# Kernel optimization log

Measured on AMD Instinct MI355X. Metric: run time of the kernel, lower is better.

Reference implementation:

```python
import jax, jax.numpy as jnp
from jax import lax
import numpy as np

T, B, H = 128, 4096, 64

def setup_inputs() -> dict:
    key = jax.random.key(0)
    ks = jax.random.split(key, 7)
    s = 1.0 / np.sqrt(H)
    Hseq = jax.random.normal(ks[0], (T, B, H), dtype=jnp.float32)
    # PyTorch nn.GRU params: weight_ih_l0 [3H,H], weight_hh_l0 [3H,H], biases [3H]; gate order r,z,n
    W_ih = jax.random.uniform(ks[1], (3 * H, H), jnp.float32, -s, s)
    W_hh = jax.random.uniform(ks[2], (3 * H, H), jnp.float32, -s, s)
    b_ih = jax.random.uniform(ks[3], (3 * H,), jnp.float32, -s, s)
    b_hh = jax.random.uniform(ks[4], (3 * H,), jnp.float32, -s, s)
    W_out = jax.random.uniform(ks[5], (1, H), jnp.float32, -s, s)
    b_out = jax.random.uniform(ks[6], (1,), jnp.float32, -s, s)
    return {"Hseq": Hseq, "W_ih": W_ih, "W_hh": W_hh, "b_ih": b_ih, "b_hh": b_hh, "W_out": W_out, "b_out": b_out}

def reference(Hseq, W_ih, W_hh, b_ih, b_hh, W_out, b_out):
    # Precompute all input-side gate projections in one big GEMM: [T,B,3H]
    x_gates = jnp.einsum('tbh,gh->tbg', Hseq, W_ih) + b_ih

    def step(h, xg):
        hg = h @ W_hh.T + b_hh                     # [B,3H]
        xr, xz, xn = jnp.split(xg, 3, axis=-1)
        hr, hz, hn = jnp.split(hg, 3, axis=-1)
        r = jax.nn.sigmoid(xr + hr)
        z = jax.nn.sigmoid(xz + hz)
        n = jnp.tanh(xn + r * hn)
        h_new = (1.0 - z) * n + z * h
        return h_new, None

    h0 = jnp.zeros(Hseq.shape[1:], Hseq.dtype)      # [B,H], PyTorch default h0=0
    last, _ = lax.scan(step, h0, x_gates)           # last hidden == Y[-1]
    return (last @ W_out.T + b_out).squeeze(-1)     # [B]
```

## Files before the change

kernel.cpp:

```cpp
#include <hip/hip_runtime.h>
#include <stdint.h>

#define TT 128
#define BB 4096
#define HH 64
#define BC 16
#define XSTR 196
#define HSTR 72

typedef __attribute__((ext_vector_type(8))) short bf16x8;
typedef __attribute__((ext_vector_type(4))) float f32x4;

static __device__ __forceinline__ short f2bf(float f) {
  uint32_t u = __builtin_bit_cast(uint32_t, f);
  u += 0x7fffu + ((u >> 16) & 1u);
  return (short)(u >> 16);
}
static __device__ __forceinline__ uint32_t cvtpk(float a, float b) {
  uint32_t r;
  asm("v_cvt_pk_bf16_f32 %0, %1, %2" : "=v"(r) : "v"(a), "v"(b));
  return r;
}
static __device__ __forceinline__ float rcpf(float x) { return __builtin_amdgcn_rcpf(x); }
static __device__ __forceinline__ float sigm(float x) { return rcpf(1.0f + __expf(-x)); }
static __device__ __forceinline__ float tanhf_fast(float x) {
  float e = __expf(2.0f * x);
  return 1.0f - 2.0f * rcpf(e + 1.0f);
}

static __device__ __forceinline__ void block_sync_lds() {
  asm volatile("" ::: "memory");
  asm volatile("s_waitcnt lgkmcnt(0)" ::: "memory");
  __builtin_amdgcn_s_barrier();
  asm volatile("" ::: "memory");
}

__global__ __launch_bounds__(512) void gru_fused(
    const float* __restrict__ Hseq, const float* __restrict__ W_ih,
    const float* __restrict__ W_hh, const float* __restrict__ b_ih,
    const float* __restrict__ b_hh, const float* __restrict__ W_out,
    const float* __restrict__ b_out, float* __restrict__ out) {
  __shared__ __align__(16) short hsh[2][BC][HSTR];
  __shared__ __align__(16) float xgsh[2][BC][XSTR];
  __shared__ float psum[4][BC];

  const int tid = threadIdx.x;
  const int w   = tid >> 6;
  const int gw  = w & 3;
  const bool cons = (w < 4);
  const int l   = tid & 63;
  const int llo = l & 15;
  const int lhi = l >> 4;
  const int k0  = lhi * 8;
  const int bbase = blockIdx.x * BC;

  for (int i = tid; i < BC * HSTR; i += 512) ((short*)hsh[0])[i] = 0;

  bf16x8 wa[3][2];
  f32x4 biasHN = {0, 0, 0, 0};
  f32x4 biasPR = {0, 0, 0, 0}, biasPZ = {0, 0, 0, 0}, biasPN = {0, 0, 0, 0};
  f32x4 hfp = {0.f, 0.f, 0.f, 0.f};
  f32x4 xq0 = {0,0,0,0}, xq1 = {0,0,0,0}, xq2 = {0,0,0,0}, xq3 = {0,0,0,0};

  if (cons) {
#pragma unroll
    for (int c = 0; c < 3; ++c) {
      const int grow = 16 * gw + 64 * c + llo;
#pragma unroll
      for (int hf = 0; hf < 2; ++hf) {
        const float* q = &W_hh[grow * 64 + hf * 32 + k0];
        bf16x8 b;
#pragma unroll
        for (int i = 0; i < 8; ++i) b[i] = f2bf(q[i]);
        wa[c][hf] = b;
      }
    }
#pragma unroll
    for (int r = 0; r < 4; ++r) biasHN[r] = b_hh[128 + 16 * gw + lhi * 4 + r];
  } else {
#pragma unroll
    for (int c = 0; c < 3; ++c) {
      const int grow = 16 * gw + 64 * c + llo;
#pragma unroll
      for (int hf = 0; hf < 2; ++hf) {
        const float* p = &W_ih[grow * 64 + hf * 32 + k0];
        bf16x8 a;
#pragma unroll
        for (int i = 0; i < 8; ++i) a[i] = f2bf(p[i]);
        wa[c][hf] = a;
      }
    }
#pragma unroll
    for (int r = 0; r < 4; ++r) {
      const int j = 16 * gw + lhi * 4 + r;
      biasPR[r] = b_ih[j] + b_hh[j];
      biasPZ[r] = b_ih[64 + j] + b_hh[64 + j];
      biasPN[r] = b_ih[128 + j];
    }
    const f32x4* p = (const f32x4*)(Hseq + (size_t)(bbase + llo) * HH + k0);
    xq0 = p[0]; xq1 = p[1]; xq2 = p[8]; xq3 = p[9];
  }

  if (!cons) {
    union { uint32_t u[4]; bf16x8 v; } c0, c1;
    c0.u[0] = cvtpk(xq0[0], xq0[1]); c0.u[1] = cvtpk(xq0[2], xq0[3]);
    c0.u[2] = cvtpk(xq1[0], xq1[1]); c0.u[3] = cvtpk(xq1[2], xq1[3]);
    c1.u[0] = cvtpk(xq2[0], xq2[1]); c1.u[1] = cvtpk(xq2[2], xq2[3]);
    c1.u[2] = cvtpk(xq3[0], xq3[1]); c1.u[3] = cvtpk(xq3[2], xq3[3]);
    f32x4 cR = biasPR, cZ = biasPZ, cN = biasPN;
    cR = __builtin_amdgcn_mfma_f32_16x16x32_bf16(wa[0][0], c0.v, cR, 0, 0, 0);
    cR = __builtin_amdgcn_mfma_f32_16x16x32_bf16(wa[0][1], c1.v, cR, 0, 0, 0);
    cZ = __builtin_amdgcn_mfma_f32_16x16x32_bf16(wa[1][0], c0.v, cZ, 0, 0, 0);
    cZ = __builtin_amdgcn_mfma_f32_16x16x32_bf16(wa[1][1], c1.v, cZ, 0, 0, 0);
    cN = __builtin_amdgcn_mfma_f32_16x16x32_bf16(wa[2][0], c0.v, cN, 0, 0, 0);
    cN = __builtin_amdgcn_mfma_f32_16x16x32_bf16(wa[2][1], c1.v, cN, 0, 0, 0);
    *(f32x4*)&xgsh[0][llo][16 * gw + lhi * 4]       = cR;
    *(f32x4*)&xgsh[0][llo][64 + 16 * gw + lhi * 4]  = cZ;
    *(f32x4*)&xgsh[0][llo][128 + 16 * gw + lhi * 4] = cN;
    const f32x4* p = (const f32x4*)(Hseq + ((size_t)BB + bbase + llo) * HH + k0);
    xq0 = p[0]; xq1 = p[1]; xq2 = p[8]; xq3 = p[9];
  }
  block_sync_lds();

  for (int t = 0; t < TT; ++t) {
    const int buf = t & 1;
    if (cons) {
      f32x4 aR  = *(const f32x4*)&xgsh[buf][llo][16 * gw + lhi * 4];
      f32x4 aZ  = *(const f32x4*)&xgsh[buf][llo][64 + 16 * gw + lhi * 4];
      f32x4 aXN = *(const f32x4*)&xgsh[buf][llo][128 + 16 * gw + lhi * 4];
      f32x4 aHN = biasHN;
      const bf16x8 hb0 = *(const bf16x8*)&hsh[buf][llo][k0];
      const bf16x8 hb1 = *(const bf16x8*)&hsh[buf][llo][k0 + 32];
      aR  = __builtin_amdgcn_mfma_f32_16x16x32_bf16(wa[0][0], hb0, aR, 0, 0, 0);
      aR  = __builtin_amdgcn_mfma_f32_16x16x32_bf16(wa[0][1], hb1, aR, 0, 0, 0);
      aZ  = __builtin_amdgcn_mfma_f32_16x16x32_bf16(wa[1][0], hb0, aZ, 0, 0, 0);
      aZ  = __builtin_amdgcn_mfma_f32_16x16x32_bf16(wa[1][1], hb1, aZ, 0, 0, 0);
      aHN = __builtin_amdgcn_mfma_f32_16x16x32_bf16(wa[2][0], hb0, aHN, 0, 0, 0);
      aHN = __builtin_amdgcn_mfma_f32_16x16x32_bf16(wa[2][1], hb1, aHN, 0, 0, 0);
#pragma unroll
      for (int r = 0; r < 4; ++r) {
        const float rr = sigm(aR[r]);
        const float zz = sigm(aZ[r]);
        const float nn = tanhf_fast(aXN[r] + rr * aHN[r]);
        hfp[r] = (1.0f - zz) * nn + zz * hfp[r];
      }
      uint2 pk;
      pk.x = cvtpk(hfp[0], hfp[1]);
      pk.y = cvtpk(hfp[2], hfp[3]);
      *(uint2*)&hsh[buf ^ 1][llo][16 * gw + lhi * 4] = pk;
    } else {
      union { uint32_t u[4]; bf16x8 v; } c0, c1;
      c0.u[0] = cvtpk(xq0[0], xq0[1]); c0.u[1] = cvtpk(xq0[2], xq0[3]);
      c0.u[2] = cvtpk(xq1[0], xq1[1]); c0.u[3] = cvtpk(xq1[2], xq1[3]);
      c1.u[0] = cvtpk(xq2[0], xq2[1]); c1.u[1] = cvtpk(xq2[2], xq2[3]);
      c1.u[2] = cvtpk(xq3[0], xq3[1]); c1.u[3] = cvtpk(xq3[2], xq3[3]);
      const int tn = (t + 2 < TT) ? t + 2 : TT - 1;
      const f32x4* p = (const f32x4*)(Hseq + ((size_t)tn * BB + bbase + llo) * HH + k0);
      xq0 = p[0]; xq1 = p[1]; xq2 = p[8]; xq3 = p[9];
      f32x4 cR = biasPR, cZ = biasPZ, cN = biasPN;
      cR = __builtin_amdgcn_mfma_f32_16x16x32_bf16(wa[0][0], c0.v, cR, 0, 0, 0);
      cR = __builtin_amdgcn_mfma_f32_16x16x32_bf16(wa[0][1], c1.v, cR, 0, 0, 0);
      cZ = __builtin_amdgcn_mfma_f32_16x16x32_bf16(wa[1][0], c0.v, cZ, 0, 0, 0);
      cZ = __builtin_amdgcn_mfma_f32_16x16x32_bf16(wa[1][1], c1.v, cZ, 0, 0, 0);
      cN = __builtin_amdgcn_mfma_f32_16x16x32_bf16(wa[2][0], c0.v, cN, 0, 0, 0);
      cN = __builtin_amdgcn_mfma_f32_16x16x32_bf16(wa[2][1], c1.v, cN, 0, 0, 0);
      const int ob = buf ^ 1;
      *(f32x4*)&xgsh[ob][llo][16 * gw + lhi * 4]       = cR;
      *(f32x4*)&xgsh[ob][llo][64 + 16 * gw + lhi * 4]  = cZ;
      *(f32x4*)&xgsh[ob][llo][128 + 16 * gw + lhi * 4] = cN;
    }
    block_sync_lds();
  }

  if (cons) {
    float part = 0.f;
#pragma unroll
    for (int r = 0; r < 4; ++r) part += hfp[r] * W_out[16 * gw + lhi * 4 + r];
    part += __shfl_xor(part, 16);
    part += __shfl_xor(part, 32);
    if (lhi == 0) psum[gw][llo] = part;
  }
  block_sync_lds();
  if (tid < BC)
    out[bbase + tid] = psum[0][tid] + psum[1][tid] + psum[2][tid] + psum[3][tid] + b_out[0];
}

extern "C" void kernel_launch(void* const* d_in, const int* in_sizes, int n_in,
                              void* d_out, int out_size, void* d_ws, size_t ws_size,
                              hipStream_t stream) {
  (void)in_sizes; (void)n_in; (void)d_ws; (void)ws_size; (void)out_size;
  const float* Hseq  = (const float*)d_in[0];
  const float* W_ih  = (const float*)d_in[1];
  const float* W_hh  = (const float*)d_in[2];
  const float* b_ih  = (const float*)d_in[3];
  const float* b_hh  = (const float*)d_in[4];
  const float* W_out = (const float*)d_in[5];
  const float* b_out = (const float*)d_in[6];
  float* out = (float*)d_out;
  gru_fused<<<BB / BC, 512, 0, stream>>>(Hseq, W_ih, W_hh, b_ih, b_hh, W_out, b_out, out);
}
```

Before: 71.42 us.

## Unroll GRU recurrence by two, deepen input prefetch, fuse gate math, raise consumer priority

The time loop is unrolled by two with constant LDS buffer indices. The producer warps now prefetch two timesteps ahead using two register sets, which hides global load latency better. The consumer gate math is rewritten so the z-sigmoid, tanh and blend collapse into a single reciprocal, with clamps to avoid overflow, which cuts transcendental and rcp count on the serial critical path. Consumer warps raise their scheduling priority with s_setprio so the latency-bound recurrence is favored over producer work. The cost is higher register pressure, and the algebraic rewrite could change numerics slightly at extreme values.

```diff
diff --git a/kernel.cpp b/kernel.cpp
--- a/kernel.cpp
+++ b/kernel.cpp
@@ -22,11 +22,6 @@
   return r;
 }
 static __device__ __forceinline__ float rcpf(float x) { return __builtin_amdgcn_rcpf(x); }
-static __device__ __forceinline__ float sigm(float x) { return rcpf(1.0f + __expf(-x)); }
-static __device__ __forceinline__ float tanhf_fast(float x) {
-  float e = __expf(2.0f * x);
-  return 1.0f - 2.0f * rcpf(e + 1.0f);
-}
 
 static __device__ __forceinline__ void block_sync_lds() {
   asm volatile("" ::: "memory");
@@ -34,6 +29,8 @@
   __builtin_amdgcn_s_barrier();
   asm volatile("" ::: "memory");
 }
+
+#define MFMA __builtin_amdgcn_mfma_f32_16x16x32_bf16
 
 __global__ __launch_bounds__(512) void gru_fused(
     const float* __restrict__ Hseq, const float* __restrict__ W_ih,
@@ -59,8 +56,6 @@
   bf16x8 wa[3][2];
   f32x4 biasHN = {0, 0, 0, 0};
   f32x4 biasPR = {0, 0, 0, 0}, biasPZ = {0, 0, 0, 0}, biasPN = {0, 0, 0, 0};
-  f32x4 hfp = {0.f, 0.f, 0.f, 0.f};
-  f32x4 xq0 = {0,0,0,0}, xq1 = {0,0,0,0}, xq2 = {0,0,0,0}, xq3 = {0,0,0,0};
 
   if (cons) {
 #pragma unroll
@@ -76,7 +71,7 @@
       }
     }
 #pragma unroll
-    for (int r = 0; r < 4; ++r) biasHN[r] = b_hh[128 + 16 * gw + lhi * 4 + r];
+    for (int r = 0; r < 4; ++r) biasHN[r] = b_hh[128 + 16 * gw + 4 * lhi + r];
   } else {
 #pragma unroll
     for (int c = 0; c < 3; ++c) {
@@ -92,90 +87,114 @@
     }
 #pragma unroll
     for (int r = 0; r < 4; ++r) {
-      const int j = 16 * gw + lhi * 4 + r;
+      const int j = 16 * gw + 4 * lhi + r;
       biasPR[r] = b_ih[j] + b_hh[j];
       biasPZ[r] = b_ih[64 + j] + b_hh[64 + j];
       biasPN[r] = b_ih[128 + j];
     }
-    const f32x4* p = (const f32x4*)(Hseq + (size_t)(bbase + llo) * HH + k0);
-    xq0 = p[0]; xq1 = p[1]; xq2 = p[8]; xq3 = p[9];
-  }
+  }
+
+  const float* xroot = Hseq + (size_t)(bbase + llo) * HH + k0;
+  f32x4 xqA0, xqA1, xqA2, xqA3, xqB0, xqB1, xqB2, xqB3;
+  f32x4 hfp = {0.f, 0.f, 0.f, 0.f};
 
   if (!cons) {
+    const f32x4* pv = (const f32x4*)xroot;
+    f32x4 q0 = pv[0], q1 = pv[1], q2 = pv[8], q3 = pv[9];
     union { uint32_t u[4]; bf16x8 v; } c0, c1;
-    c0.u[0] = cvtpk(xq0[0], xq0[1]); c0.u[1] = cvtpk(xq0[2], xq0[3]);
-    c0.u[2] = cvtpk(xq1[0], xq1[1]); c0.u[3] = cvtpk(xq1[2], xq1[3]);
-    c1.u[0] = cvtpk(xq2[0], xq2[1]); c1.u[1] = cvtpk(xq2[2], xq2[3]);
-    c1.u[2] = cvtpk(xq3[0], xq3[1]); c1.u[3] = cvtpk(xq3[2], xq3[3]);
+    c0.u[0] = cvtpk(q0[0], q0[1]); c0.u[1] = cvtpk(q0[2], q0[3]);
+    c0.u[2] = cvtpk(q1[0], q1[1]); c0.u[3] = cvtpk(q1[2], q1[3]);
+    c1.u[0] = cvtpk(q2[0], q2[1]); c1.u[1] = cvtpk(q2[2], q2[3]);
+    c1.u[2] = cvtpk(q3[0], q3[1]); c1.u[3] = cvtpk(q3[2], q3[3]);
     f32x4 cR = biasPR, cZ = biasPZ, cN = biasPN;
-    cR = __builtin_amdgcn_mfma_f32_16x16x32_bf16(wa[0][0], c0.v, cR, 0, 0, 0);
-    cR = __builtin_amdgcn_mfma_f32_16x16x32_bf16(wa[0][1], c1.v, cR, 0, 0, 0);
-    cZ = __builtin_amdgcn_mfma_f32_16x16x32_bf16(wa[1][0], c0.v, cZ, 0, 0, 0);
-    cZ = __builtin_amdgcn_mfma_f32_16x16x32_bf16(wa[1][1], c1.v, cZ, 0, 0, 0);
-    cN = __builtin_amdgcn_mfma_f32_16x16x32_bf16(wa[2][0], c0.v, cN, 0, 0, 0);
-    cN = __builtin_amdgcn_mfma_f32_16x16x32_bf16(wa[2][1], c1.v, cN, 0, 0, 0);
-    *(f32x4*)&xgsh[0][llo][16 * gw + lhi * 4]       = cR;
-    *(f32x4*)&xgsh[0][llo][64 + 16 * gw + lhi * 4]  = cZ;
-    *(f32x4*)&xgsh[0][llo][128 + 16 * gw + lhi * 4] = cN;
-    const f32x4* p = (const f32x4*)(Hseq + ((size_t)BB + bbase + llo) * HH + k0);
-    xq0 = p[0]; xq1 = p[1]; xq2 = p[8]; xq3 = p[9];
+    cR = MFMA(wa[0][0], c0.v, cR, 0, 0, 0);
+    cR = MFMA(wa[0][1], c1.v, cR, 0, 0, 0);
+    cZ = MFMA(wa[1][0], c0.v, cZ, 0, 0, 0);
+    cZ = MFMA(wa[1][1], c1.v, cZ, 0, 0, 0);
+    cN = MFMA(wa[2][0], c0.v, cN, 0, 0, 0);
+    cN = MFMA(wa[2][1], c1.v, cN, 0, 0, 0);
+    *(f32x4*)&xgsh[0][llo][16 * gw + 4 * lhi]       = cR;
+    *(f32x4*)&xgsh[0][llo][64 + 16 * gw + 4 * lhi]  = cZ;
+    *(f32x4*)&xgsh[0][llo][128 + 16 * gw + 4 * lhi] = cN;
+    const f32x4* pa = (const f32x4*)(xroot + (size_t)1 * BB * HH);
+    xqA0 = pa[0]; xqA1 = pa[1]; xqA2 = pa[8]; xqA3 = pa[9];
+    const f32x4* pb = (const f32x4*)(xroot + (size_t)2 * BB * HH);
+    xqB0 = pb[0]; xqB1 = pb[1]; xqB2 = pb[8]; xqB3 = pb[9];
   }
   block_sync_lds();
 
-  for (int t = 0; t < TT; ++t) {
-    const int buf = t & 1;
-    if (cons) {
-      f32x4 aR  = *(const f32x4*)&xgsh[buf][llo][16 * gw + lhi * 4];
-      f32x4 aZ  = *(const f32x4*)&xgsh[buf][llo][64 + 16 * gw + lhi * 4];
-      f32x4 aXN = *(const f32x4*)&xgsh[buf][llo][128 + 16 * gw + lhi * 4];
-      f32x4 aHN = biasHN;
-      const bf16x8 hb0 = *(const bf16x8*)&hsh[buf][llo][k0];
-      const bf16x8 hb1 = *(const bf16x8*)&hsh[buf][llo][k0 + 32];
-      aR  = __builtin_amdgcn_mfma_f32_16x16x32_bf16(wa[0][0], hb0, aR, 0, 0, 0);
-      aR  = __builtin_amdgcn_mfma_f32_16x16x32_bf16(wa[0][1], hb1, aR, 0, 0, 0);
-      aZ  = __builtin_amdgcn_mfma_f32_16x16x32_bf16(wa[1][0], hb0, aZ, 0, 0, 0);
-      aZ  = __builtin_amdgcn_mfma_f32_16x16x32_bf16(wa[1][1], hb1, aZ, 0, 0, 0);
-      aHN = __builtin_amdgcn_mfma_f32_16x16x32_bf16(wa[2][0], hb0, aHN, 0, 0, 0);
-      aHN = __builtin_amdgcn_mfma_f32_16x16x32_bf16(wa[2][1], hb1, aHN, 0, 0, 0);
-#pragma unroll
-      for (int r = 0; r < 4; ++r) {
-        const float rr = sigm(aR[r]);
-        const float zz = sigm(aZ[r]);
-        const float nn = tanhf_fast(aXN[r] + rr * aHN[r]);
-        hfp[r] = (1.0f - zz) * nn + zz * hfp[r];
-      }
-      uint2 pk;
-      pk.x = cvtpk(hfp[0], hfp[1]);
-      pk.y = cvtpk(hfp[2], hfp[3]);
-      *(uint2*)&hsh[buf ^ 1][llo][16 * gw + lhi * 4] = pk;
-    } else {
-      union { uint32_t u[4]; bf16x8 v; } c0, c1;
-      c0.u[0] = cvtpk(xq0[0], xq0[1]); c0.u[1] = cvtpk(xq0[2], xq0[3]);
-      c0.u[2] = cvtpk(xq1[0], xq1[1]); c0.u[3] = cvtpk(xq1[2], xq1[3]);
-      c1.u[0] = cvtpk(xq2[0], xq2[1]); c1.u[1] = cvtpk(xq2[2], xq2[3]);
-      c1.u[2] = cvtpk(xq3[0], xq3[1]); c1.u[3] = cvtpk(xq3[2], xq3[3]);
-      const int tn = (t + 2 < TT) ? t + 2 : TT - 1;
-      const f32x4* p = (const f32x4*)(Hseq + ((size_t)tn * BB + bbase + llo) * HH + k0);
-      xq0 = p[0]; xq1 = p[1]; xq2 = p[8]; xq3 = p[9];
-      f32x4 cR = biasPR, cZ = biasPZ, cN = biasPN;
-      cR = __builtin_amdgcn_mfma_f32_16x16x32_bf16(wa[0][0], c0.v, cR, 0, 0, 0);
-      cR = __builtin_amdgcn_mfma_f32_16x16x32_bf16(wa[0][1], c1.v, cR, 0, 0, 0);
-      cZ = __builtin_amdgcn_mfma_f32_16x16x32_bf16(wa[1][0], c0.v, cZ, 0, 0, 0);
-      cZ = __builtin_amdgcn_mfma_f32_16x16x32_bf16(wa[1][1], c1.v, cZ, 0, 0, 0);
-      cN = __builtin_amdgcn_mfma_f32_16x16x32_bf16(wa[2][0], c0.v, cN, 0, 0, 0);
-      cN = __builtin_amdgcn_mfma_f32_16x16x32_bf16(wa[2][1], c1.v, cN, 0, 0, 0);
-      const int ob = buf ^ 1;
-      *(f32x4*)&xgsh[ob][llo][16 * gw + lhi * 4]       = cR;
-      *(f32x4*)&xgsh[ob][llo][64 + 16 * gw + lhi * 4]  = cZ;
-      *(f32x4*)&xgsh[ob][llo][128 + 16 * gw + lhi * 4] = cN;
-    }
+#define CSTEP(RB, WB)                                                         \
+  {                                                                           \
+    __builtin_amdgcn_s_setprio(1);                                            \
+    const bf16x8 hb0 = *(const bf16x8*)&hsh[RB][llo][k0];                     \
+    const bf16x8 hb1 = *(const bf16x8*)&hsh[RB][llo][k0 + 32];                \
+    f32x4 aR = *(const f32x4*)&xgsh[RB][llo][16 * gw + 4 * lhi];              \
+    aR = MFMA(wa[0][0], hb0, aR, 0, 0, 0);                                    \
+    aR = MFMA(wa[0][1], hb1, aR, 0, 0, 0);                                    \
+    f32x4 aZ  = *(const f32x4*)&xgsh[RB][llo][64 + 16 * gw + 4 * lhi];        \
+    f32x4 aXN = *(const f32x4*)&xgsh[RB][llo][128 + 16 * gw + 4 * lhi];       \
+    aZ  = MFMA(wa[1][0], hb0, aZ, 0, 0, 0);                                   \
+    aZ  = MFMA(wa[1][1], hb1, aZ, 0, 0, 0);                                   \
+    f32x4 aHN = MFMA(wa[2][0], hb0, biasHN, 0, 0, 0);                         \
+    aHN = MFMA(wa[2][1], hb1, aHN, 0, 0, 0);                                  \
+    _Pragma("unroll")                                                         \
+    for (int r = 0; r < 4; ++r) {                                             \
+      const float u  = __expf(-aR[r]);                                        \
+      const float az = fminf(30.f, fmaxf(-30.f, aZ[r]));                      \
+      const float t  = __expf(-az);                                           \
+      const float rr = rcpf(1.0f + u);                                        \
+      float c = aXN[r] + rr * aHN[r];                                         \
+      c = fminf(15.f, fmaxf(-15.f, c));                                       \
+      const float s   = __expf(2.0f * c);                                     \
+      const float qq  = s + 1.0f;                                             \
+      const float num = t * (s - 1.0f) + hfp[r] * qq;                         \
+      const float den = qq * (1.0f + t);                                      \
+      hfp[r] = num * rcpf(den);                                               \
+    }                                                                         \
+    uint2 pk;                                                                 \
+    pk.x = cvtpk(hfp[0], hfp[1]);                                             \
+    pk.y = cvtpk(hfp[2], hfp[3]);                                             \
+    *(uint2*)&hsh[WB][llo][16 * gw + 4 * lhi] = pk;                           \
+    __builtin_amdgcn_s_setprio(0);                                            \
+  }
+
+#define PSTEP(OB, XQ0, XQ1, XQ2, XQ3, TN)                                     \
+  {                                                                           \
+    union { uint32_t u[4]; bf16x8 v; } c0, c1;                                \
+    c0.u[0] = cvtpk(XQ0[0], XQ0[1]); c0.u[1] = cvtpk(XQ0[2], XQ0[3]);         \
+    c0.u[2] = cvtpk(XQ1[0], XQ1[1]); c0.u[3] = cvtpk(XQ1[2], XQ1[3]);         \
+    c1.u[0] = cvtpk(XQ2[0], XQ2[1]); c1.u[1] = cvtpk(XQ2[2], XQ2[3]);         \
+    c1.u[2] = cvtpk(XQ3[0], XQ3[1]); c1.u[3] = cvtpk(XQ3[2], XQ3[3]);         \
+    {                                                                         \
+      const int tn = (TN) < TT ? (TN) : (TT - 1);                             \
+      const f32x4* pv = (const f32x4*)(xroot + (size_t)tn * BB * HH);         \
+      XQ0 = pv[0]; XQ1 = pv[1]; XQ2 = pv[8]; XQ3 = pv[9];                     \
+    }                                                                         \
+    f32x4 cR = biasPR, cZ = biasPZ, cN = biasPN;                              \
+    cR = MFMA(wa[0][0], c0.v, cR, 0, 0, 0);                                   \
+    cR = MFMA(wa[0][1], c1.v, cR, 0, 0, 0);                                   \
+    cZ = MFMA(wa[1][0], c0.v, cZ, 0, 0, 0);                                   \
+    cZ = MFMA(wa[1][1], c1.v, cZ, 0, 0, 0);                                   \
+    cN = MFMA(wa[2][0], c0.v, cN, 0, 0, 0);                                   \
+    cN = MFMA(wa[2][1], c1.v, cN, 0, 0, 0);                                   \
+    *(f32x4*)&xgsh[OB][llo][16 * gw + 4 * lhi]       = cR;                    \
+    *(f32x4*)&xgsh[OB][llo][64 + 16 * gw + 4 * lhi]  = cZ;                    \
+    *(f32x4*)&xgsh[OB][llo][128 + 16 * gw + 4 * lhi] = cN;                    \
+  }
+
+  for (int t = 0; t < TT; t += 2) {
+    if (cons) { CSTEP(0, 1) } else { PSTEP(1, xqA0, xqA1, xqA2, xqA3, t + 3) }
     block_sync_lds();
-  }
+    if (cons) { CSTEP(1, 0) } else { PSTEP(0, xqB0, xqB1, xqB2, xqB3, t + 4) }
+    block_sync_lds();
+  }
+#undef CSTEP
+#undef PSTEP
 
   if (cons) {
     float part = 0.f;
 #pragma unroll
-    for (int r = 0; r < 4; ++r) part += hfp[r] * W_out[16 * gw + lhi * 4 + r];
+    for (int r = 0; r < 4; ++r) part += hfp[r] * W_out[16 * gw + 4 * lhi + r];
     part += __shfl_xor(part, 16);
     part += __shfl_xor(part, 32);
     if (lhi == 0) psum[gw][llo] = part;
```

Measured after the change: 70.72 us. About the same (-1.0%).
